# Optimization experiments

Hardware: AMD Instinct MI355X
Metric: run time of the kernel (lower is better)

Reference implementation:

```python
import jax, jax.numpy as jnp
import numpy as np

B, C, LQ, D = 4096, 64, 32, 128
H = 192  # 1.5 * dim
MARGIN = 1.0
EPS = 1e-12


def l2norm(x):
    return x * jax.lax.rsqrt(jnp.maximum(jnp.sum(x * x, axis=1, keepdims=True), EPS))


def setup_inputs() -> dict:
    key = jax.random.key(0)
    ks = jax.random.split(key, 16)
    question_word_embs = jax.random.normal(ks[0], (B, LQ, D), jnp.float32)
    question_lengths = jax.random.randint(ks[1], (B,), 1, LQ + 1, jnp.int32)
    header_embs = jax.random.normal(ks[2], (B, C, D), jnp.float32)
    table_word_embs = jax.random.normal(ks[3], (B, C, D), jnp.float32)
    num_cols = jax.random.randint(ks[4], (B,), 1, C + 1, jnp.int32)
    masks = (jnp.arange(C)[None, :] < num_cols[:, None]).astype(jnp.float32)
    labels = (jax.random.uniform(ks[5], (B,)) < 0.5).astype(jnp.float32)
    # table_encoder_dense: Dense(1.5*dim, relu) -> Dense(dim, relu)
    W1 = jax.random.normal(ks[6], (2 * D, H), jnp.float32) / np.sqrt(2 * D)
    b1 = jnp.zeros((H,), jnp.float32)
    W2 = jax.random.normal(ks[7], (H, D), jnp.float32) / np.sqrt(H)
    b2 = jnp.zeros((D,), jnp.float32)
    # query LSTM(dim, activation='relu'): gate order i, f, c, o (Keras)
    Wx = jax.random.normal(ks[8], (D, 4 * D), jnp.float32) / np.sqrt(D)
    Wh = jax.random.normal(ks[9], (D, 4 * D), jnp.float32) / np.sqrt(D)
    b_lstm = jnp.zeros((4 * D,), jnp.float32)
    return dict(question_word_embs=question_word_embs, question_lengths=question_lengths,
                header_embs=header_embs, table_word_embs=table_word_embs,
                num_cols=num_cols, masks=masks, labels=labels,
                W1=W1, b1=b1, W2=W2, b2=b2, Wx=Wx, Wh=Wh, b_lstm=b_lstm)


def masked_lstm(x, lengths, Wx, Wh, b):
    # x: [B, L, D]; returns final hidden state at each row's true length
    xs = jnp.transpose(x, (1, 0, 2))  # [L, B, D]
    h0 = jnp.zeros((x.shape[0], D), x.dtype)
    c0 = jnp.zeros_like(h0)

    def step(carry, inp):
        h, c = carry
        t, x_t = inp
        z = x_t @ Wx + h @ Wh + b  # [B, 4D]
        i, f, g, o = jnp.split(z, 4, axis=1)
        i = jax.nn.sigmoid(i)
        f = jax.nn.sigmoid(f)
        g = jax.nn.relu(g)           # activation='relu'
        o = jax.nn.sigmoid(o)
        c_new = f * c + i * g
        h_new = o * jax.nn.relu(c_new)
        m = (t < lengths)[:, None].astype(x_t.dtype)
        return (m * h_new + (1 - m) * h, m * c_new + (1 - m) * c), None

    (h, _), _ = jax.lax.scan(step, (h0, c0), (jnp.arange(xs.shape[0]), xs))
    return h


def reference(question_word_embs, question_lengths, header_embs, table_word_embs,
              num_cols, masks, labels, W1, b1, W2, b2, Wx, Wh, b_lstm):
    # ---- table path ----
    flat = jnp.concatenate([header_embs.reshape(-1, D), table_word_embs.reshape(-1, D)], axis=1)  # [B*C, 2D]
    h = jax.nn.relu(flat @ W1 + b1)
    te = jax.nn.relu(h @ W2 + b2).reshape(B, C, D)
    te = te * masks[:, :, None]
    te = jnp.sum(te, axis=1) / num_cols.astype(jnp.float32)[:, None]
    te = l2norm(te)
    # ---- query path (ragged-word LSTM encoder) ----
    qe = masked_lstm(question_word_embs, question_lengths, Wx, Wh, b_lstm)
    qe = l2norm(qe)
    # ---- contrastive loss ----
    d = jnp.sum(jnp.square(qe - te), axis=1)
    d_sqrt = jnp.sqrt(d)
    loss = labels * d + (1.0 - labels) * jnp.square(jnp.maximum(0.0, MARGIN - d_sqrt))
    return 0.5 * jnp.mean(loss)
```

## Files before the change

kernel.cpp:

```cpp
#include <hip/hip_runtime.h>
#include <math.h>

#define B_  4096
#define C_  64
#define LQ_ 32
#define D_  128
#define H_  192

typedef __attribute__((ext_vector_type(8))) short bf16x8;
typedef __attribute__((ext_vector_type(4))) float f32x4;

#define KEEP(x) asm volatile("" : "+v"(x))

__device__ inline unsigned cvt_pk_bf16(float lo, float hi) {
    unsigned r;
    asm("v_cvt_pk_bf16_f32 %0, %1, %2" : "=v"(r) : "v"(lo), "v"(hi));
    return r;
}
__device__ inline short f2b(float x) { return (short)(cvt_pk_bf16(x, x) & 0xffff); }
__device__ inline float sigm(float x) { return 1.f / (1.f + __expf(-x)); }

__global__ __launch_bounds__(256) void prep_kernel(
    const float* __restrict__ W1, const float* __restrict__ W2,
    const float* __restrict__ Wx, const float* __restrict__ Wh,
    short* __restrict__ W1T, short* __restrict__ W2T, short* __restrict__ WTl)
{
    int idx = blockIdx.x * 256 + threadIdx.x;
    if (idx < 192 * 256) {
        int j = idx >> 8, k = idx & 255;
        W1T[idx] = f2b(W1[k * H_ + j]);
    }
    if (idx < 128 * 192) {
        int j = idx / 192, k = idx - j * 192;
        W2T[idx] = f2b(W2[k * D_ + j]);
    }
    if (idx < 512 * 256) {
        int p = idx >> 8, k = idx & 255;
        int w = p >> 6, g = (p >> 4) & 3, jj = p & 15;
        int jo = g * 128 + w * 16 + jj;
        float v = (k < 128) ? Wx[k * 512 + jo] : Wh[(k - 128) * 512 + jo];
        WTl[idx] = f2b(v);
    }
}

__global__ __launch_bounds__(512) __attribute__((amdgpu_waves_per_eu(2, 2)))
void table_kernel(
    const float* __restrict__ header, const float* __restrict__ tword,
    const float* __restrict__ masks, const int* __restrict__ num_cols,
    const short* __restrict__ W1T, const float* __restrict__ b1,
    const short* __restrict__ W2T, const float* __restrict__ b2,
    float* __restrict__ te_out)
{
    const int bb0 = blockIdx.x * 16;
    const int tid = threadIdx.x;
    const int w   = tid >> 6;
    const int l   = tid & 63;
    const int lg  = l >> 4;
    const int ln  = l & 15;
    const int ww  = w & 3;
    const int wr  = w >> 2;

    __shared__ __align__(16) short flat_s[2][32 * 256];
    __shared__ __align__(16) short h_s[32 * 192];
    __shared__ float msk[64];
    __shared__ float redv[8][128];
    __shared__ float redq[2];

    bf16x8 bw1[3][8];
    float bias1[3];
    #pragma unroll
    for (int ct = 0; ct < 3; ++ct) {
        int j = ww * 48 + ct * 16 + ln;
        bias1[ct] = b1[j];
        #pragma unroll
        for (int ks = 0; ks < 8; ++ks)
            bw1[ct][ks] = *(const bf16x8*)&W1T[j * 256 + ks * 32 + lg * 8];
    }
    bf16x8 bw2[2][6];
    float bias2[2];
    #pragma unroll
    for (int ct = 0; ct < 2; ++ct) {
        int j = ww * 32 + ct * 16 + ln;
        bias2[ct] = b2[j];
        #pragma unroll
        for (int ks = 0; ks < 6; ++ks)
            bw2[ct][ks] = *(const bf16x8*)&W2T[j * 192 + ks * 32 + lg * 8];
    }
    #pragma unroll
    for (int ct = 0; ct < 3; ++ct) {
        KEEP(bias1[ct]);
        #pragma unroll
        for (int ks = 0; ks < 8; ++ks) KEEP(bw1[ct][ks]);
    }
    #pragma unroll
    for (int ct = 0; ct < 2; ++ct) {
        KEEP(bias2[ct]);
        #pragma unroll
        for (int ks = 0; ks < 6; ++ks) KEEP(bw2[ct][ks]);
    }

    float4 pf[4];
    auto issue = [&](int cc) {
        int b    = bb0 + (cc >> 1);
        int row0 = (cc & 1) * 32;
        #pragma unroll
        for (int i = 0; i < 4; ++i) {
            int idx = i * 512 + tid;
            int r   = idx >> 6;
            int c   = idx & 63;
            const float* src = (c < 32)
                ? &header[((size_t)b * C_ + row0 + r) * D_ + c * 4]
                : &tword [((size_t)b * C_ + row0 + r) * D_ + (c - 32) * 4];
            pf[i] = *(const float4*)src;
        }
    };
    issue(0);

    float csum0 = 0.f, csum1 = 0.f;

    for (int cc = 0; cc < 32; ++cc) {
        const int b    = bb0 + (cc >> 1);
        const int half = cc & 1;
        char* fbuf = (char*)flat_s[cc & 1];

        #pragma unroll
        for (int i = 0; i < 4; ++i) {
            int idx = i * 512 + tid;
            int r   = idx >> 6;
            int c   = idx & 63;
            uint2 p;
            p.x = cvt_pk_bf16(pf[i].x, pf[i].y);
            p.y = cvt_pk_bf16(pf[i].z, pf[i].w);
            *(uint2*)(fbuf + r * 512 + ((c * 8) ^ ((r & 7) << 4))) = p;
        }
        if (cc + 1 < 32) issue(cc + 1);
        if (half == 0 && tid < 64) msk[tid] = masks[b * C_ + tid];
        __syncthreads();

        {
            int row = wr * 16 + ln;
            bf16x8 a[8];
            #pragma unroll
            for (int ks = 0; ks < 8; ++ks)
                a[ks] = *(const bf16x8*)(fbuf + row * 512 +
                                         ((ks * 64 + lg * 16) ^ ((row & 7) << 4)));
            f32x4 acc[3];
            #pragma unroll
            for (int ct = 0; ct < 3; ++ct)
                acc[ct] = (f32x4){bias1[ct], bias1[ct], bias1[ct], bias1[ct]};
            #pragma unroll
            for (int ks = 0; ks < 8; ++ks)
                #pragma unroll
                for (int ct = 0; ct < 3; ++ct)
                    acc[ct] = __builtin_amdgcn_mfma_f32_16x16x32_bf16(a[ks], bw1[ct][ks], acc[ct], 0, 0, 0);
            #pragma unroll
            for (int ct = 0; ct < 3; ++ct) {
                int col = ww * 48 + ct * 16 + ln;
                #pragma unroll
                for (int reg = 0; reg < 4; ++reg) {
                    int orow = wr * 16 + lg * 4 + reg;
                    *(short*)((char*)h_s + orow * 384 + ((col * 2) ^ ((orow & 7) << 4))) =
                        f2b(fmaxf(acc[ct][reg], 0.f));
                }
            }
        }
        __syncthreads();

        {
            int row = wr * 16 + ln;
            bf16x8 a[6];
            #pragma unroll
            for (int ks = 0; ks < 6; ++ks)
                a[ks] = *(const bf16x8*)((char*)h_s + row * 384 +
                                         ((ks * 64 + lg * 16) ^ ((row & 7) << 4)));
            f32x4 acc2[2];
            #pragma unroll
            for (int ct = 0; ct < 2; ++ct)
                acc2[ct] = (f32x4){bias2[ct], bias2[ct], bias2[ct], bias2[ct]};
            #pragma unroll
            for (int ks = 0; ks < 6; ++ks)
                #pragma unroll
                for (int ct = 0; ct < 2; ++ct)
                    acc2[ct] = __builtin_amdgcn_mfma_f32_16x16x32_bf16(a[ks], bw2[ct][ks], acc2[ct], 0, 0, 0);
            #pragma unroll
            for (int reg = 0; reg < 4; ++reg) {
                int crow = half * 32 + wr * 16 + lg * 4 + reg;
                float m = msk[crow];
                csum0 = fmaf(fmaxf(acc2[0][reg], 0.f), m, csum0);
                csum1 = fmaf(fmaxf(acc2[1][reg], 0.f), m, csum1);
            }
        }

        if (half == 1) {
            #pragma unroll
            for (int s = 16; s < 64; s <<= 1) {
                csum0 += __shfl_xor(csum0, s, 64);
                csum1 += __shfl_xor(csum1, s, 64);
            }
            if (l < 16) {
                redv[w][ww * 32 + ln]      = csum0;
                redv[w][ww * 32 + 16 + ln] = csum1;
            }
            __syncthreads();
            float v = 0.f;
            if (tid < 128) {
                int j   = tid;
                int wwj = j >> 5;
                v = (redv[wwj][j] + redv[wwj + 4][j]) / (float)num_cols[b];
                float s = v * v;
                #pragma unroll
                for (int sh = 1; sh < 64; sh <<= 1) s += __shfl_xor(s, sh, 64);
                if (l == 0) redq[w] = s;
            }
            __syncthreads();
            if (tid < 128) {
                float inv = rsqrtf(fmaxf(redq[0] + redq[1], 1e-12f));
                te_out[(size_t)b * D_ + tid] = v * inv;
            }
            csum0 = 0.f; csum1 = 0.f;
        }
    }
}

__global__ __launch_bounds__(512) __attribute__((amdgpu_waves_per_eu(2, 2)))
void lstm_kernel(
    const float* __restrict__ q, const int* __restrict__ lengths,
    const short* __restrict__ WTl, const float* __restrict__ bl,
    float* __restrict__ qe_out)
{
    const int tid = threadIdx.x;
    const int b0  = blockIdx.x * 16;
    const int w   = tid >> 6;
    const int l   = tid & 63;
    const int lg  = l >> 4;
    const int ln  = l & 15;
    const int d0  = w * 16 + lg * 4;

    __shared__ __align__(16) short xh[2][16 * 256];
    __shared__ float red8[8][16];

    bf16x8 wf[4][8];
    #pragma unroll
    for (int g = 0; g < 4; ++g)
        #pragma unroll
        for (int ks = 0; ks < 8; ++ks)
            wf[g][ks] = *(const bf16x8*)&WTl[(w * 64 + g * 16 + ln) * 256 + ks * 32 + lg * 8];
    float bias[4][4];
    #pragma unroll
    for (int g = 0; g < 4; ++g)
        #pragma unroll
        for (int reg = 0; reg < 4; ++reg)
            bias[g][reg] = bl[g * 128 + d0 + reg];
    #pragma unroll
    for (int g = 0; g < 4; ++g) {
        #pragma unroll
        for (int ks = 0; ks < 8; ++ks) KEEP(wf[g][ks]);
        #pragma unroll
        for (int reg = 0; reg < 4; ++reg) KEEP(bias[g][reg]);
    }

    float creg[4] = {0.f, 0.f, 0.f, 0.f};
    float hreg[4] = {0.f, 0.f, 0.f, 0.f};
    const int len = lengths[b0 + ln];
    const int sr = tid >> 5, sc = tid & 31;

    float4 qv = *(const float4*)&q[((size_t)(b0 + sr) * LQ_ + 0) * D_ + sc * 4];

    for (int t = 0; t < LQ_; ++t) {
        char* buf = (char*)xh[t & 1];
        uint2 px; px.x = cvt_pk_bf16(qv.x, qv.y); px.y = cvt_pk_bf16(qv.z, qv.w);
        *(uint2*)(buf + sr * 512 + ((sc * 8) ^ ((sr & 7) << 4))) = px;
        uint2 ph; ph.x = cvt_pk_bf16(hreg[0], hreg[1]); ph.y = cvt_pk_bf16(hreg[2], hreg[3]);
        *(uint2*)(buf + ln * 512 + ((256 + d0 * 2) ^ ((ln & 7) << 4))) = ph;
        if (t + 1 < LQ_)
            qv = *(const float4*)&q[((size_t)(b0 + sr) * LQ_ + (t + 1)) * D_ + sc * 4];
        __syncthreads();

        bf16x8 xf[8];
        #pragma unroll
        for (int ks = 0; ks < 8; ++ks)
            xf[ks] = *(const bf16x8*)(buf + ln * 512 + ((ks * 64 + lg * 16) ^ ((ln & 7) << 4)));
        f32x4 acc[4];
        #pragma unroll
        for (int g = 0; g < 4; ++g)
            acc[g] = (f32x4){bias[g][0], bias[g][1], bias[g][2], bias[g][3]};
        #pragma unroll
        for (int ks = 0; ks < 8; ++ks)
            #pragma unroll
            for (int g = 0; g < 4; ++g)
                acc[g] = __builtin_amdgcn_mfma_f32_16x16x32_bf16(wf[g][ks], xf[ks], acc[g], 0, 0, 0);

        bool live = (t < len);
        #pragma unroll
        for (int reg = 0; reg < 4; ++reg) {
            float iv = sigm(acc[0][reg]);
            float fv = sigm(acc[1][reg]);
            float gv = fmaxf(acc[2][reg], 0.f);
            float ov = sigm(acc[3][reg]);
            float cn = fmaf(fv, creg[reg], iv * gv);
            float hn = ov * fmaxf(cn, 0.f);
            if (live) { creg[reg] = cn; hreg[reg] = hn; }
        }
    }

    float sq = 0.f;
    #pragma unroll
    for (int reg = 0; reg < 4; ++reg) sq = fmaf(hreg[reg], hreg[reg], sq);
    sq += __shfl_xor(sq, 16, 64);
    sq += __shfl_xor(sq, 32, 64);
    if (l < 16) red8[w][ln] = sq;
    __syncthreads();
    float tot = 0.f;
    #pragma unroll
    for (int ww = 0; ww < 8; ++ww) tot += red8[ww][ln];
    float inv = rsqrtf(fmaxf(tot, 1e-12f));
    float4 o;
    o.x = hreg[0] * inv; o.y = hreg[1] * inv; o.z = hreg[2] * inv; o.w = hreg[3] * inv;
    *(float4*)&qe_out[(size_t)(b0 + ln) * D_ + d0] = o;
}

__global__ __launch_bounds__(64) void loss_kernel(
    const float* __restrict__ te, const float* __restrict__ qe,
    const float* __restrict__ labels, float* __restrict__ partial)
{
    const int tid = threadIdx.x;
    const int b   = blockIdx.x * 64 + tid;
    float dsum = 0.f;
    #pragma unroll 8
    for (int k4 = 0; k4 < 32; ++k4) {
        float4 a = *(const float4*)&qe[(size_t)b * D_ + k4 * 4];
        float4 c = *(const float4*)&te[(size_t)b * D_ + k4 * 4];
        float dx = a.x - c.x, dy = a.y - c.y, dz = a.z - c.z, dw = a.w - c.w;
        dsum += dx * dx + dy * dy + dz * dz + dw * dw;
    }
    float lab = labels[b];
    float ds  = sqrtf(dsum);
    float ml  = fmaxf(0.f, 1.f - ds);
    float loss = lab * dsum + (1.f - lab) * ml * ml;
    #pragma unroll
    for (int s = 32; s > 0; s >>= 1) loss += __shfl_xor(loss, s, 64);
    if (tid == 0) partial[blockIdx.x] = loss;
}

__global__ void final_kernel(const float* __restrict__ partial, float* __restrict__ out)
{
    const int tid = threadIdx.x;
    float v = partial[tid];
    #pragma unroll
    for (int s = 32; s > 0; s >>= 1) v += __shfl_xor(v, s, 64);
    if (tid == 0) out[0] = 0.5f * v / (float)B_;
}

extern "C" void kernel_launch(void* const* d_in, const int* in_sizes, int n_in,
                              void* d_out, int out_size, void* d_ws, size_t ws_size,
                              hipStream_t stream)
{
    const float* q      = (const float*)d_in[0];
    const int*   qlen   = (const int*)d_in[1];
    const float* header = (const float*)d_in[2];
    const float* tword  = (const float*)d_in[3];
    const int*   ncols  = (const int*)d_in[4];
    const float* masks  = (const float*)d_in[5];
    const float* labels = (const float*)d_in[6];
    const float* W1     = (const float*)d_in[7];
    const float* b1     = (const float*)d_in[8];
    const float* W2     = (const float*)d_in[9];
    const float* b2     = (const float*)d_in[10];
    const float* Wx     = (const float*)d_in[11];
    const float* Wh     = (const float*)d_in[12];
    const float* bl     = (const float*)d_in[13];
    float* out = (float*)d_out;

    float* te      = (float*)d_ws;
    float* qe      = te + (size_t)B_ * D_;
    float* partial = qe + (size_t)B_ * D_;
    short* W1T     = (short*)(partial + 64);
    short* W2T     = W1T + 192 * 256;
    short* WTl     = W2T + 128 * 192;

    prep_kernel<<<512, 256, 0, stream>>>(W1, W2, Wx, Wh, W1T, W2T, WTl);
    table_kernel<<<B_ / 16, 512, 0, stream>>>(header, tword, masks, ncols, W1T, b1, W2T, b2, te);
    lstm_kernel<<<B_ / 16, 512, 0, stream>>>(q, qlen, WTl, bl, qe);
    loss_kernel<<<B_ / 64, 64, 0, stream>>>(te, qe, labels, partial);
    final_kernel<<<1, 64, 0, stream>>>(partial, out);
}
```

Measured before the change: 166.7 us.

## Use LDS-only barriers, preload masks, and stream A-fragments per k-step

Replaces __syncthreads with a custom barrier that waits only on LDS counters (lgkmcnt), so outstanding global prefetch loads are no longer drained at each barrier. All masks and num_cols for the block are loaded into shared memory once up front instead of per batch inside the loop. A-fragment LDS reads now happen one k-step at a time to cut register pressure, and waves_per_eu is relaxed to (1,2). The risk is that the weaker barrier is unsafe if any global-memory dependency between threads relied on the full wait.

```diff
diff --git a/kernel.cpp b/kernel.cpp
--- a/kernel.cpp
+++ b/kernel.cpp
@@ -19,6 +19,12 @@
 }
 __device__ inline short f2b(float x) { return (short)(cvt_pk_bf16(x, x) & 0xffff); }
 __device__ inline float sigm(float x) { return 1.f / (1.f + __expf(-x)); }
+
+__device__ inline void wg_barrier() {
+    asm volatile("s_waitcnt lgkmcnt(0)" ::: "memory");
+    __builtin_amdgcn_s_barrier();
+    asm volatile("" ::: "memory");
+}
 
 __global__ __launch_bounds__(256) void prep_kernel(
     const float* __restrict__ W1, const float* __restrict__ W2,
@@ -43,7 +49,7 @@
     }
 }
 
-__global__ __launch_bounds__(512) __attribute__((amdgpu_waves_per_eu(2, 2)))
+__global__ __launch_bounds__(512) __attribute__((amdgpu_waves_per_eu(1, 2)))
 void table_kernel(
     const float* __restrict__ header, const float* __restrict__ tword,
     const float* __restrict__ masks, const int* __restrict__ num_cols,
@@ -62,7 +68,8 @@
 
     __shared__ __align__(16) short flat_s[2][32 * 256];
     __shared__ __align__(16) short h_s[32 * 192];
-    __shared__ float msk[64];
+    __shared__ float msk_s[16][64];
+    __shared__ float ncol_s[16];
     __shared__ float redv[8][128];
     __shared__ float redq[2];
 
@@ -98,6 +105,13 @@
         #pragma unroll
         for (int ks = 0; ks < 6; ++ks) KEEP(bw2[ct][ks]);
     }
+
+    {
+        int i0 = tid * 2;
+        *(float2*)&((float*)msk_s)[i0] = *(const float2*)&masks[(size_t)bb0 * C_ + i0];
+        if (tid < 16) ncol_s[tid] = (float)num_cols[bb0 + tid];
+    }
+    __syncthreads();
 
     float4 pf[4];
     auto issue = [&](int cc) {
@@ -119,7 +133,7 @@
     float csum0 = 0.f, csum1 = 0.f;
 
     for (int cc = 0; cc < 32; ++cc) {
-        const int b    = bb0 + (cc >> 1);
+        const int bi   = cc >> 1;
         const int half = cc & 1;
         char* fbuf = (char*)flat_s[cc & 1];
 
@@ -134,25 +148,22 @@
             *(uint2*)(fbuf + r * 512 + ((c * 8) ^ ((r & 7) << 4))) = p;
         }
         if (cc + 1 < 32) issue(cc + 1);
-        if (half == 0 && tid < 64) msk[tid] = masks[b * C_ + tid];
-        __syncthreads();
+        wg_barrier();
 
         {
             int row = wr * 16 + ln;
-            bf16x8 a[8];
-            #pragma unroll
-            for (int ks = 0; ks < 8; ++ks)
-                a[ks] = *(const bf16x8*)(fbuf + row * 512 +
-                                         ((ks * 64 + lg * 16) ^ ((row & 7) << 4)));
             f32x4 acc[3];
             #pragma unroll
             for (int ct = 0; ct < 3; ++ct)
                 acc[ct] = (f32x4){bias1[ct], bias1[ct], bias1[ct], bias1[ct]};
             #pragma unroll
-            for (int ks = 0; ks < 8; ++ks)
+            for (int ks = 0; ks < 8; ++ks) {
+                bf16x8 a = *(const bf16x8*)(fbuf + row * 512 +
+                                            ((ks * 64 + lg * 16) ^ ((row & 7) << 4)));
                 #pragma unroll
                 for (int ct = 0; ct < 3; ++ct)
-                    acc[ct] = __builtin_amdgcn_mfma_f32_16x16x32_bf16(a[ks], bw1[ct][ks], acc[ct], 0, 0, 0);
+                    acc[ct] = __builtin_amdgcn_mfma_f32_16x16x32_bf16(a, bw1[ct][ks], acc[ct], 0, 0, 0);
+            }
             #pragma unroll
             for (int ct = 0; ct < 3; ++ct) {
                 int col = ww * 48 + ct * 16 + ln;
@@ -164,28 +175,26 @@
                 }
             }
         }
-        __syncthreads();
+        wg_barrier();
 
         {
             int row = wr * 16 + ln;
-            bf16x8 a[6];
-            #pragma unroll
-            for (int ks = 0; ks < 6; ++ks)
-                a[ks] = *(const bf16x8*)((char*)h_s + row * 384 +
-                                         ((ks * 64 + lg * 16) ^ ((row & 7) << 4)));
             f32x4 acc2[2];
             #pragma unroll
             for (int ct = 0; ct < 2; ++ct)
                 acc2[ct] = (f32x4){bias2[ct], bias2[ct], bias2[ct], bias2[ct]};
             #pragma unroll
-            for (int ks = 0; ks < 6; ++ks)
+            for (int ks = 0; ks < 6; ++ks) {
+                bf16x8 a = *(const bf16x8*)((char*)h_s + row * 384 +
+                                            ((ks * 64 + lg * 16) ^ ((row & 7) << 4)));
                 #pragma unroll
                 for (int ct = 0; ct < 2; ++ct)
-                    acc2[ct] = __builtin_amdgcn_mfma_f32_16x16x32_bf16(a[ks], bw2[ct][ks], acc2[ct], 0, 0, 0);
+                    acc2[ct] = __builtin_amdgcn_mfma_f32_16x16x32_bf16(a, bw2[ct][ks], acc2[ct], 0, 0, 0);
+            }
             #pragma unroll
             for (int reg = 0; reg < 4; ++reg) {
                 int crow = half * 32 + wr * 16 + lg * 4 + reg;
-                float m = msk[crow];
+                float m = msk_s[bi][crow];
                 csum0 = fmaf(fmaxf(acc2[0][reg], 0.f), m, csum0);
                 csum1 = fmaf(fmaxf(acc2[1][reg], 0.f), m, csum1);
             }
@@ -201,28 +210,28 @@
                 redv[w][ww * 32 + ln]      = csum0;
                 redv[w][ww * 32 + 16 + ln] = csum1;
             }
-            __syncthreads();
+            wg_barrier();
             float v = 0.f;
             if (tid < 128) {
                 int j   = tid;
                 int wwj = j >> 5;
-                v = (redv[wwj][j] + redv[wwj + 4][j]) / (float)num_cols[b];
+                v = (redv[wwj][j] + redv[wwj + 4][j]) / ncol_s[bi];
                 float s = v * v;
                 #pragma unroll
                 for (int sh = 1; sh < 64; sh <<= 1) s += __shfl_xor(s, sh, 64);
                 if (l == 0) redq[w] = s;
             }
-            __syncthreads();
+            wg_barrier();
             if (tid < 128) {
                 float inv = rsqrtf(fmaxf(redq[0] + redq[1], 1e-12f));
-                te_out[(size_t)b * D_ + tid] = v * inv;
+                te_out[(size_t)(bb0 + bi) * D_ + tid] = v * inv;
             }
             csum0 = 0.f; csum1 = 0.f;
         }
     }
 }
 
-__global__ __launch_bounds__(512) __attribute__((amdgpu_waves_per_eu(2, 2)))
+__global__ __launch_bounds__(512) __attribute__((amdgpu_waves_per_eu(1, 2)))
 void lstm_kernel(
     const float* __restrict__ q, const int* __restrict__ lengths,
     const short* __restrict__ WTl, const float* __restrict__ bl,
@@ -274,21 +283,19 @@
         *(uint2*)(buf + ln * 512 + ((256 + d0 * 2) ^ ((ln & 7) << 4))) = ph;
         if (t + 1 < LQ_)
             qv = *(const float4*)&q[((size_t)(b0 + sr) * LQ_ + (t + 1)) * D_ + sc * 4];
-        __syncthreads();
-
-        bf16x8 xf[8];
-        #pragma unroll
-        for (int ks = 0; ks < 8; ++ks)
-            xf[ks] = *(const bf16x8*)(buf + ln * 512 + ((ks * 64 + lg * 16) ^ ((ln & 7) << 4)));
+        wg_barrier();
+
         f32x4 acc[4];
         #pragma unroll
         for (int g = 0; g < 4; ++g)
             acc[g] = (f32x4){bias[g][0], bias[g][1], bias[g][2], bias[g][3]};
         #pragma unroll
-        for (int ks = 0; ks < 8; ++ks)
+        for (int ks = 0; ks < 8; ++ks) {
+            bf16x8 xf = *(const bf16x8*)(buf + ln * 512 + ((ks * 64 + lg * 16) ^ ((ln & 7) << 4)));
             #pragma unroll
             for (int g = 0; g < 4; ++g)
-                acc[g] = __builtin_amdgcn_mfma_f32_16x16x32_bf16(wf[g][ks], xf[ks], acc[g], 0, 0, 0);
+                acc[g] = __builtin_amdgcn_mfma_f32_16x16x32_bf16(wf[g][ks], xf, acc[g], 0, 0, 0);
+        }
 
         bool live = (t < len);
         #pragma unroll
@@ -309,7 +316,7 @@
     sq += __shfl_xor(sq, 16, 64);
     sq += __shfl_xor(sq, 32, 64);
     if (l < 16) red8[w][ln] = sq;
-    __syncthreads();
+    wg_barrier();
     float tot = 0.f;
     #pragma unroll
     for (int ww = 0; ww < 8; ++ww) tot += red8[ww][ln];
```

Measured after the change: 136.3 us. 1.22x faster.
